# Kernel tuning notes

Measured on AMD Instinct MI355X. Metric: run time of the kernel, lower is better.

The kernel has to match this reference:

```python
import jax, jax.numpy as jnp
import numpy as np

B, S, E, H = 2, 4096, 512, 8
DK = E // H


def setup_inputs() -> dict:
    k = jax.random.key(0)
    ks = jax.random.split(k, 11)
    sc = 0.02
    return {
        "query": jax.random.normal(ks[0], (B, S, E), jnp.float32),
        "key_in": jax.random.normal(ks[1], (B, S, E), jnp.float32),
        "value": jax.random.normal(ks[2], (B, S, E), jnp.float32),
        "Wq": jax.random.normal(ks[3], (E, E), jnp.float32) * sc,
        "bq": jax.random.normal(ks[4], (E,), jnp.float32) * sc,
        "Wk": jax.random.normal(ks[5], (E, E), jnp.float32) * sc,
        "bk": jax.random.normal(ks[6], (E,), jnp.float32) * sc,
        "Wv": jax.random.normal(ks[7], (E, E), jnp.float32) * sc,
        "bv": jax.random.normal(ks[8], (E,), jnp.float32) * sc,
        "Wo": jax.random.normal(ks[9], (E, E), jnp.float32) * sc,
        "bo": jax.random.normal(ks[10], (E,), jnp.float32) * sc,
    }


def reference(query, key_in, value, Wq, bq, Wk, bk, Wv, bv, Wo, bo):
    b, s, _ = query.shape
    # Linear projections
    q = query @ Wq + bq
    k = key_in @ Wk + bk
    v = value @ Wv + bv
    # [b, s, H, dk] -> [b, H, s, dk]
    q = q.reshape(b, s, H, DK).transpose(0, 2, 1, 3)
    k = k.reshape(b, s, H, DK).transpose(0, 2, 1, 3)
    v = v.reshape(b, s, H, DK).transpose(0, 2, 1, 3)
    # NOTE: source bug — softmax over UNSCALED scores (1/sqrt scaling in the
    # original is applied to a dead variable after softmax). Reproduce faithfully.
    scores = jnp.einsum("bhqd,bhkd->bhqk", q, k)  # [b,H,s,s] — O(N^2) materialized
    weights = jax.nn.softmax(scores.astype(jnp.float32), axis=-1)
    attn = jnp.einsum("bhqk,bhkd->bhqd", weights, v)
    # [b,H,s,dk] -> [b,s,E]
    concat = attn.transpose(0, 2, 1, 3).reshape(b, s, E)
    return concat @ Wo + bo
```

## Files before the change

kernel.cpp:

```cpp
#include <hip/hip_runtime.h>
#include <hip/hip_bf16.h>

#define B_  2
#define S_  4096
#define E_  512
#define H_  8
#define DK_ 64
#define M_  8192

typedef float f32x4  __attribute__((ext_vector_type(4)));
typedef float f32x16 __attribute__((ext_vector_type(16)));
typedef short s16x8  __attribute__((ext_vector_type(8)));
typedef short s16x4  __attribute__((ext_vector_type(4)));

static __device__ __forceinline__ short f2bf(float x) {
  __hip_bfloat16 h = __float2bfloat16(x);
  return __builtin_bit_cast(short, h);
}

static __device__ __forceinline__ f32x4 mfma32(s16x8 a, s16x8 b, f32x4 c) {
  return __builtin_amdgcn_mfma_f32_16x16x32_bf16(a, b, c, 0, 0, 0);
}

static __device__ __forceinline__ f32x16 mfma3232(s16x8 a, s16x8 b, f32x16 c) {
  return __builtin_amdgcn_mfma_f32_32x32x16_bf16(a, b, c, 0, 0, 0);
}

static __device__ __forceinline__ float fastexp2(float x) {
#if __has_builtin(__builtin_amdgcn_exp2f)
  return __builtin_amdgcn_exp2f(x);
#else
  return __expf(x * 0.69314718056f);
#endif
}

static __device__ __forceinline__ void gload_lds16(const void* g, void* l) {
  __builtin_amdgcn_global_load_lds(
      (const __attribute__((address_space(1))) unsigned int*)g,
      (__attribute__((address_space(3))) unsigned int*)l, 16, 0, 0);
}

__global__ __launch_bounds__(256) void conv_bf16_all(
    const float* __restrict__ q, const float* __restrict__ k,
    const float* __restrict__ v, short* __restrict__ out, int n4) {
  const float* in = (blockIdx.y == 0) ? q : ((blockIdx.y == 1) ? k : v);
  short* o = out + (size_t)blockIdx.y * (size_t)n4 * 4;
  int i = blockIdx.x * 256 + threadIdx.x;
  if (i < n4) {
    float4 x = *((const float4*)in + i);
    s16x4 r;
    r[0] = f2bf(x.x); r[1] = f2bf(x.y); r[2] = f2bf(x.z); r[3] = f2bf(x.w);
    *((s16x4*)o + i) = r;
  }
}

__global__ __launch_bounds__(256) void conv_wT_all(
    const float* __restrict__ Wq, const float* __restrict__ Wk,
    const float* __restrict__ Wv, const float* __restrict__ Wo,
    short* __restrict__ Wt) {
  const float* W = (blockIdx.y == 0) ? Wq
                   : ((blockIdx.y == 1) ? Wk : ((blockIdx.y == 2) ? Wv : Wo));
  short* o = Wt + (size_t)blockIdx.y * (E_ * E_);
  int idx = blockIdx.x * 256 + threadIdx.x;
  int j = idx >> 9, k = idx & 511;
  o[idx] = f2bf(W[(size_t)k * E_ + j]);
}

static __device__ __forceinline__ void gemm_core_512(
    const short* __restrict__ A, const short* __restrict__ Bt,
    short* As, short* Bs, int tm, int tn, f32x4 acc[4][4]) {
  const int tid = threadIdx.x;
  const int wave = tid >> 6, lane = tid & 63;
  const int wm = (wave >> 1) * 64, wn = (wave & 1) * 64;
  const int c = lane & 15, g = lane >> 4;
  for (int kk = 0; kk < 512; kk += 64) {
#pragma unroll
    for (int i = 0; i < 4; ++i) {
      int ob = wave * 4096 + i * 1024 + lane * 16;
      int row = ob >> 7;
      int col = (ob & 127) >> 1;
      gload_lds16(A + (size_t)(tm + row) * 512 + kk + col,
                  (char*)As + wave * 4096 + i * 1024);
      gload_lds16(Bt + (size_t)(tn + row) * 512 + kk + col,
                  (char*)Bs + wave * 4096 + i * 1024);
    }
    __syncthreads();
#pragma unroll
    for (int s = 0; s < 2; ++s) {
      s16x8 af[4], bfr[4];
#pragma unroll
      for (int i = 0; i < 4; ++i)
        af[i] = *(const s16x8*)&As[(wm + i * 16 + c) * 64 + s * 32 + g * 8];
#pragma unroll
      for (int j = 0; j < 4; ++j)
        bfr[j] = *(const s16x8*)&Bs[(wn + j * 16 + c) * 64 + s * 32 + g * 8];
#pragma unroll
      for (int i = 0; i < 4; ++i)
#pragma unroll
        for (int j = 0; j < 4; ++j)
          acc[i][j] = mfma32(af[i], bfr[j], acc[i][j]);
    }
    __syncthreads();
  }
}

__global__ __launch_bounds__(256) void gemm_qkv(
    const short* __restrict__ Xq, const short* __restrict__ Xk,
    const short* __restrict__ Xv, const short* __restrict__ Wt,
    const float* __restrict__ bq, const float* __restrict__ bk,
    const float* __restrict__ bv,
    short* __restrict__ Qo, short* __restrict__ Ko, short* __restrict__ Vto) {
  __shared__ __align__(16) short As[128 * 64];
  __shared__ __align__(16) short Bs[128 * 64];
  const int z = blockIdx.z;
  const short* A = (z == 0) ? Xq : ((z == 1) ? Xk : Xv);
  const short* Bt = Wt + z * (E_ * E_);
  const float* bias = (z == 0) ? bq : ((z == 1) ? bk : bv);
  const int tm = blockIdx.x * 128, tn = blockIdx.y * 128;
  f32x4 acc[4][4] = {};
  gemm_core_512(A, Bt, As, Bs, tm, tn, acc);

  const int tid = threadIdx.x;
  const int wave = tid >> 6, lane = tid & 63;
  const int wm = (wave >> 1) * 64, wn = (wave & 1) * 64;
  const int c = lane & 15, g = lane >> 4;
#pragma unroll
  for (int i = 0; i < 4; ++i) {
#pragma unroll
    for (int j = 0; j < 4; ++j) {
      const int gc = tn + wn + j * 16 + c;
      const float bb = bias[gc];
      const int h = gc >> 6, dk = gc & 63;
#pragma unroll
      for (int r = 0; r < 4; ++r) {
        const int gr = tm + wm + i * 16 + g * 4 + r;
        const int b = gr >> 12, s = gr & 4095;
        float v = acc[i][j][r] + bb;
        if (z == 0) v *= 1.44269504f;
        const short hv = f2bf(v);
        if (z == 2)
          Vto[(size_t)((b * H_ + h) * DK_ + dk) * S_ + s] = hv;
        else if (z == 1)
          Ko[(size_t)((b * H_ + h) * S_ + s) * DK_ + dk] = hv;
        else
          Qo[(size_t)((b * H_ + h) * S_ + s) * DK_ + dk] = hv;
      }
    }
  }
}

__global__ __launch_bounds__(256) void gemm_out(
    const short* __restrict__ AO, const short* __restrict__ Wot,
    const float* __restrict__ bo, float* __restrict__ out) {
  __shared__ __align__(16) short As[128 * 64];
  __shared__ __align__(16) short Bs[128 * 64];
  const int tm = blockIdx.x * 128, tn = blockIdx.y * 128;
  f32x4 acc[4][4] = {};
  gemm_core_512(AO, Wot, As, Bs, tm, tn, acc);

  const int tid = threadIdx.x;
  const int wave = tid >> 6, lane = tid & 63;
  const int wm = (wave >> 1) * 64, wn = (wave & 1) * 64;
  const int c = lane & 15, g = lane >> 4;
#pragma unroll
  for (int i = 0; i < 4; ++i) {
#pragma unroll
    for (int j = 0; j < 4; ++j) {
      const int gc = tn + wn + j * 16 + c;
      const float bb = bo[gc];
#pragma unroll
      for (int r = 0; r < 4; ++r) {
        const int gr = tm + wm + i * 16 + g * 4 + r;
        out[(size_t)gr * E_ + gc] = acc[i][j][r] + bb;
      }
    }
  }
}

__global__ __launch_bounds__(256, 2) void attn_fwd(
    const short* __restrict__ Q, const short* __restrict__ K,
    const short* __restrict__ Vt, short* __restrict__ O) {
  __shared__ __align__(16) short Ks[2][64 * 64];
  __shared__ __align__(16) short Vs[4][64 * 64];
  const int tid = threadIdx.x;
  const int wave = tid >> 6, lane = tid & 63;
  const int qi = lane & 31, hi = lane >> 5;
  const int bh = blockIdx.y;
  const int b = bh >> 3, h = bh & 7;
  const int q0 = blockIdx.x * 128 + wave * 32;
  const short* Qp = Q + (size_t)bh * S_ * DK_;
  const short* Kp = K + (size_t)bh * S_ * DK_;
  const short* Vp = Vt + (size_t)bh * DK_ * S_;

  s16x8 qf[4];
#pragma unroll
  for (int s = 0; s < 4; ++s)
    qf[s] = *(const s16x8*)(Qp + (size_t)(q0 + qi) * DK_ + s * 16 + hi * 8);

  f32x16 o0 = {}, o1 = {};
  f32x16 lacc = {};
  s16x8 ones;
#pragma unroll
  for (int e = 0; e < 8; ++e) ones[e] = (short)0x3F80;

  int kOffL[2], vOffL[2];
#pragma unroll
  for (int r = 0; r < 2; ++r) {
    const int j = wave * 2 + r;
    const int row = (j >> 2) * 32 + qi;
    const int srow = (row & 32) | ((row & 8) << 1) | ((row & 4) << 1) |
                     ((row & 16) >> 2) | (row & 3);
    kOffL[r] = srow * DK_ + (j & 3) * 16 + hi * 8;
    vOffL[r] = ((j >> 2) * 32 + qi) * S_ + ((j >> 1) & 1) * 32 +
               (j & 1) * 16 + hi * 8;
  }

  auto stage = [&](int kt) {
#pragma unroll
    for (int r = 0; r < 2; ++r) {
      const int j = wave * 2 + r;
      gload_lds16(Kp + (size_t)kt * 64 * DK_ + kOffL[r],
                  (char*)Ks[kt & 1] + j * 1024);
      gload_lds16(Vp + (size_t)kt * 64 + vOffL[r],
                  (char*)Vs[kt & 3] + j * 1024);
    }
  };

  const int lb = lane << 4;

  auto qk = [&](const short* Kbuf, f32x16& s0, f32x16& s1) {
    const char* Kc = (const char*)Kbuf + lb;
    f32x16 t0 = {}, t1 = {};
    __builtin_amdgcn_s_setprio(1);
#pragma unroll
    for (int s = 0; s < 4; ++s) {
      s16x8 ka = *(const s16x8*)(Kc + s * 1024);
      s16x8 kb = *(const s16x8*)(Kc + 4096 + s * 1024);
      t0 = mfma3232(ka, qf[s], t0);
      t1 = mfma3232(kb, qf[s], t1);
    }
    __builtin_amdgcn_s_setprio(0);
    s0 = t0; s1 = t1;
  };

  auto softpv = [&](const f32x16& s0, const f32x16& s1, const short* Vbuf) {
    const char* Vc = (const char*)Vbuf + lb;
    float p0[16], p1[16];
#pragma unroll
    for (int r = 0; r < 16; ++r) { p0[r] = fastexp2(s0[r]); p1[r] = fastexp2(s1[r]); }
    s16x8 pb[2][2];
#pragma unroll
    for (int ks = 0; ks < 2; ++ks)
#pragma unroll
      for (int j = 0; j < 8; ++j) {
        const int r = (j & 3) | (ks << 2) | ((j >> 2) << 3);
        pb[0][ks][j] = f2bf(p0[r]);
        pb[1][ks][j] = f2bf(p1[r]);
      }
    __builtin_amdgcn_s_setprio(1);
#pragma unroll
    for (int hf = 0; hf < 2; ++hf)
#pragma unroll
      for (int ks = 0; ks < 2; ++ks) {
        s16x8 va0 = *(const s16x8*)(Vc + (hf * 2 + ks) * 1024);
        s16x8 va1 = *(const s16x8*)(Vc + 4096 + (hf * 2 + ks) * 1024);
        o0 = mfma3232(va0, pb[hf][ks], o0);
        o1 = mfma3232(va1, pb[hf][ks], o1);
        lacc = mfma3232(ones, pb[hf][ks], lacc);
      }
    __builtin_amdgcn_s_setprio(0);
  };

  const int NT = S_ / 64;
  f32x16 sA0, sA1, sB0, sB1;

  stage(0);
  __syncthreads();
  stage(1);
  qk(Ks[0], sA0, sA1);
  __syncthreads();

  for (int t = 0; t < NT; t += 2) {
    if (t + 2 < NT) stage(t + 2);
    qk(Ks[(t + 1) & 1], sB0, sB1);
    softpv(sA0, sA1, Vs[t & 3]);
    __syncthreads();
    if (t + 3 < NT) stage(t + 3);
    if (t + 2 < NT) qk(Ks[(t + 2) & 1], sA0, sA1);
    softpv(sB0, sB1, Vs[(t + 1) & 3]);
    __syncthreads();
  }

  const float rl = 1.f / lacc[0];
  short* Op = O + ((size_t)(b * S_ + q0 + qi)) * E_ + h * DK_;
#pragma unroll
  for (int rr = 0; rr < 4; ++rr) {
    s16x4 ov0, ov1;
#pragma unroll
    for (int e = 0; e < 4; ++e) {
      ov0[e] = f2bf(o0[rr * 4 + e] * rl);
      ov1[e] = f2bf(o1[rr * 4 + e] * rl);
    }
    *(s16x4*)(Op + rr * 8 + hi * 4) = ov0;
    *(s16x4*)(Op + 32 + rr * 8 + hi * 4) = ov1;
  }
}

extern "C" void kernel_launch(void* const* d_in, const int* in_sizes, int n_in,
                              void* d_out, int out_size, void* d_ws, size_t ws_size,
                              hipStream_t stream) {
  const float* query  = (const float*)d_in[0];
  const float* key_in = (const float*)d_in[1];
  const float* value  = (const float*)d_in[2];
  const float* Wq = (const float*)d_in[3];
  const float* bq = (const float*)d_in[4];
  const float* Wk = (const float*)d_in[5];
  const float* bk = (const float*)d_in[6];
  const float* Wv = (const float*)d_in[7];
  const float* bv = (const float*)d_in[8];
  const float* Wo = (const float*)d_in[9];
  const float* bo = (const float*)d_in[10];
  float* out = (float*)d_out;

  const size_t NA = (size_t)M_ * E_;
  short* ws  = (short*)d_ws;
  short* Xq  = ws;
  short* Wt  = Xq + 3 * NA;
  short* Wot = Wt + 3 * E_ * E_;
  short* Qb  = Wt + 4 * E_ * E_;
  short* Kb  = Qb + NA;
  short* Vtb = Kb + NA;
  short* AO  = Vtb + NA;
  short* Xk  = Xq + NA;
  short* Xv  = Xk + NA;

  conv_bf16_all<<<dim3(NA / 1024, 3), 256, 0, stream>>>(
      query, key_in, value, Xq, (int)(NA / 4));
  conv_wT_all<<<dim3(E_ * E_ / 256, 4), 256, 0, stream>>>(Wq, Wk, Wv, Wo, Wt);

  gemm_qkv<<<dim3(M_ / 128, E_ / 128, 3), 256, 0, stream>>>(
      Xq, Xk, Xv, Wt, bq, bk, bv, Qb, Kb, Vtb);
  attn_fwd<<<dim3(S_ / 128, B_ * H_), 256, 0, stream>>>(Qb, Kb, Vtb, AO);
  gemm_out<<<dim3(M_ / 128, E_ / 128), 256, 0, stream>>>(AO, Wot, bo, out);
}
```

Baseline: 167.8 us.

## Split attention waves into two phase-offset roles in a 512-thread block

The attention kernel grows to 8 waves covering 256 queries per block, so each K/V tile staged in LDS is shared by twice as many queries. The per-wave two-tile software pipeline is replaced by two wave groups running half a step apart: one group does QK then softmax·V on each tile, the other does the previous tile's softmax·V before the current QK. The intent is to overlap exp/softmax work of one group with the MFMA work of the other while cutting K/V global traffic, and V buffering drops to three slots. The cost is that launch_bounds(512,2) tightens the register budget, which risks spills, and each wave loses its own QK/softmax interleave.

```diff
diff --git a/kernel.cpp b/kernel.cpp
--- a/kernel.cpp
+++ b/kernel.cpp
@@ -177,17 +177,18 @@
   }
 }
 
-__global__ __launch_bounds__(256, 2) void attn_fwd(
+__global__ __launch_bounds__(512, 2) void attn_fwd(
     const short* __restrict__ Q, const short* __restrict__ K,
     const short* __restrict__ Vt, short* __restrict__ O) {
   __shared__ __align__(16) short Ks[2][64 * 64];
-  __shared__ __align__(16) short Vs[4][64 * 64];
+  __shared__ __align__(16) short Vs[3][64 * 64];
   const int tid = threadIdx.x;
   const int wave = tid >> 6, lane = tid & 63;
+  const int role = wave >> 2;
   const int qi = lane & 31, hi = lane >> 5;
   const int bh = blockIdx.y;
   const int b = bh >> 3, h = bh & 7;
-  const int q0 = blockIdx.x * 128 + wave * 32;
+  const int q0 = blockIdx.x * 256 + wave * 32;
   const short* Qp = Q + (size_t)bh * S_ * DK_;
   const short* Kp = K + (size_t)bh * S_ * DK_;
   const short* Vp = Vt + (size_t)bh * DK_ * S_;
@@ -203,27 +204,22 @@
 #pragma unroll
   for (int e = 0; e < 8; ++e) ones[e] = (short)0x3F80;
 
-  int kOffL[2], vOffL[2];
-#pragma unroll
-  for (int r = 0; r < 2; ++r) {
-    const int j = wave * 2 + r;
+  int kOff, vOff;
+  {
+    const int j = wave;
     const int row = (j >> 2) * 32 + qi;
     const int srow = (row & 32) | ((row & 8) << 1) | ((row & 4) << 1) |
                      ((row & 16) >> 2) | (row & 3);
-    kOffL[r] = srow * DK_ + (j & 3) * 16 + hi * 8;
-    vOffL[r] = ((j >> 2) * 32 + qi) * S_ + ((j >> 1) & 1) * 32 +
-               (j & 1) * 16 + hi * 8;
+    kOff = srow * DK_ + (j & 3) * 16 + hi * 8;
+    vOff = ((j >> 2) * 32 + qi) * S_ + ((j >> 1) & 1) * 32 +
+           (j & 1) * 16 + hi * 8;
   }
 
   auto stage = [&](int kt) {
-#pragma unroll
-    for (int r = 0; r < 2; ++r) {
-      const int j = wave * 2 + r;
-      gload_lds16(Kp + (size_t)kt * 64 * DK_ + kOffL[r],
-                  (char*)Ks[kt & 1] + j * 1024);
-      gload_lds16(Vp + (size_t)kt * 64 + vOffL[r],
-                  (char*)Vs[kt & 3] + j * 1024);
-    }
+    gload_lds16(Kp + (size_t)kt * 64 * DK_ + kOff,
+                (char*)Ks[kt & 1] + wave * 1024);
+    gload_lds16(Vp + (size_t)kt * 64 + vOff,
+                (char*)Vs[kt % 3] + wave * 1024);
   };
 
   const int lb = lane << 4;
@@ -272,24 +268,23 @@
   };
 
   const int NT = S_ / 64;
-  f32x16 sA0, sA1, sB0, sB1;
+  f32x16 sp0, sp1;
 
   stage(0);
   __syncthreads();
-  stage(1);
-  qk(Ks[0], sA0, sA1);
-  __syncthreads();
-
-  for (int t = 0; t < NT; t += 2) {
-    if (t + 2 < NT) stage(t + 2);
-    qk(Ks[(t + 1) & 1], sB0, sB1);
-    softpv(sA0, sA1, Vs[t & 3]);
+
+  for (int t = 0; t < NT; ++t) {
+    if (t + 1 < NT) stage(t + 1);
+    if (role == 0) {
+      qk(Ks[t & 1], sp0, sp1);
+      softpv(sp0, sp1, Vs[t % 3]);
+    } else {
+      if (t > 0) softpv(sp0, sp1, Vs[(t - 1) % 3]);
+      qk(Ks[t & 1], sp0, sp1);
+    }
     __syncthreads();
-    if (t + 3 < NT) stage(t + 3);
-    if (t + 2 < NT) qk(Ks[(t + 2) & 1], sA0, sA1);
-    softpv(sB0, sB1, Vs[(t + 1) & 3]);
-    __syncthreads();
-  }
+  }
+  if (role == 1) softpv(sp0, sp1, Vs[(NT - 1) % 3]);
 
   const float rl = 1.f / lacc[0];
   short* Op = O + ((size_t)(b * S_ + q0 + qi)) * E_ + h * DK_;
@@ -340,6 +335,6 @@
 
   gemm_qkv<<<dim3(M_ / 128, E_ / 128, 3), 256, 0, stream>>>(
       Xq, Xk, Xv, Wt, bq, bk, bv, Qb, Kb, Vtb);
-  attn_fwd<<<dim3(S_ / 128, B_ * H_), 256, 0, stream>>>(Qb, Kb, Vtb, AO);
+  attn_fwd<<<dim3(S_ / 256, B_ * H_), 512, 0, stream>>>(Qb, Kb, Vtb, AO);
   gemm_out<<<dim3(M_ / 128, E_ / 128), 256, 0, stream>>>(AO, Wot, bo, out);
 }
```

New measurement: 168.5 us. Within noise of the previous version (+0.4%).
